# Performance work log

Measured on AMD Instinct MI355X. Metric: run time of the kernel, lower is better.

## Reference

```python
import jax, jax.numpy as jnp
import numpy as np

N = 100000
D_IN = 64
D_HID = 64


def _sage_conv(x, edge_index, Wl, bl, Wr):
    # PyG SAGEConv (mean aggr): out = lin_l(mean_j x_j) + lin_r(x_root)
    src, dst = edge_index[0], edge_index[1]
    n = x.shape[0]
    msg_sum = jax.ops.segment_sum(x[src], dst, num_segments=n)  # [N, d]
    deg = jax.ops.segment_sum(jnp.ones_like(src, dtype=x.dtype), dst, num_segments=n)
    agg = msg_sum / jnp.maximum(deg, 1.0)[:, None]
    return agg @ Wl + bl + x @ Wr


def setup_inputs() -> dict:
    key = jax.random.key(0)
    ks = jax.random.split(key, 8)
    x = jax.random.normal(ks[0], (N, D_IN), dtype=jnp.float32)
    edge_index = jax.random.randint(ks[1], (2, 16 * N), 0, N, dtype=jnp.int64)
    s = 1.0 / np.sqrt(D_IN)
    W1l = jax.random.uniform(ks[2], (D_IN, D_HID), minval=-s, maxval=s, dtype=jnp.float32)
    b1 = jnp.zeros((D_HID,), dtype=jnp.float32)
    W1r = jax.random.uniform(ks[3], (D_IN, D_HID), minval=-s, maxval=s, dtype=jnp.float32)
    s2 = 1.0 / np.sqrt(D_HID)
    W2l = jax.random.uniform(ks[4], (D_HID, D_HID), minval=-s2, maxval=s2, dtype=jnp.float32)
    b2 = jnp.zeros((D_HID,), dtype=jnp.float32)
    W2r = jax.random.uniform(ks[5], (D_HID, D_HID), minval=-s2, maxval=s2, dtype=jnp.float32)
    Wc = jax.random.uniform(ks[6], (D_HID, 2), minval=-s2, maxval=s2, dtype=jnp.float32)
    bc = jax.random.uniform(ks[7], (2,), minval=-s2, maxval=s2, dtype=jnp.float32)
    return {"x": x, "edge_index": edge_index, "W1l": W1l, "b1": b1, "W1r": W1r,
            "W2l": W2l, "b2": b2, "W2r": W2r, "Wc": Wc, "bc": bc}


def reference(x, edge_index, W1l, b1, W1r, W2l, b2, W2r, Wc, bc):
    h = jax.nn.relu(_sage_conv(x, edge_index, W1l, b1, W1r))
    h = _sage_conv(h, edge_index, W2l, b2, W2r)
    return h @ Wc + bc  # [N, 2] logits
```

## Files before the change

### kernel.cpp

```cpp
#include <hip/hip_runtime.h>


#define SCAN_BS 1024
#define BUCKET_BITS 7
#define BUCKET_NODES 128
#define NBUCK_MAX 1024
#define EPB 8192

__global__ void __launch_bounds__(256) bucket_hist_kernel(const int* __restrict__ dst,
                                                          int* __restrict__ counts,
                                                          int ne, int B, int NB) {
  __shared__ int hist[NBUCK_MAX];
  for (int k = threadIdx.x; k < B; k += 256) hist[k] = 0;
  __syncthreads();
  int base = blockIdx.x * EPB;
#pragma unroll 4
  for (int i = 0; i < EPB / 256; ++i) {
    int e = base + i * 256 + threadIdx.x;
    if (e < ne) atomicAdd(&hist[dst[e] >> BUCKET_BITS], 1);
  }
  __syncthreads();
  for (int k = threadIdx.x; k < B; k += 256) counts[k * NB + blockIdx.x] = hist[k];
}

__device__ __forceinline__ int block_scan_inclusive_1024(int v, int* wsums) {
  int lane = threadIdx.x & 63;
  int wid = threadIdx.x >> 6;
  int s = v;
#pragma unroll
  for (int off = 1; off < 64; off <<= 1) {
    int t = __shfl_up(s, off);
    if (lane >= off) s += t;
  }
  if (lane == 63) wsums[wid] = s;
  __syncthreads();
  if (wid == 0) {
    int ws = (lane < 16) ? wsums[lane] : 0;
#pragma unroll
    for (int off = 1; off < 16; off <<= 1) {
      int t = __shfl_up(ws, off);
      if (lane >= off) ws += t;
    }
    if (lane < 16) wsums[lane] = ws;
  }
  __syncthreads();
  if (wid > 0) s += wsums[wid - 1];
  return s;
}

__global__ void __launch_bounds__(SCAN_BS) scan_a_inplace_kernel(int* __restrict__ data,
                                                                 int* __restrict__ bsums,
                                                                 int S) {
  __shared__ int wsums[16];
  int i = blockIdx.x * SCAN_BS + threadIdx.x;
  int v = (i < S) ? data[i] : 0;
  int inc = block_scan_inclusive_1024(v, wsums);
  if (i < S) data[i] = inc - v;
  if (threadIdx.x == SCAN_BS - 1) bsums[blockIdx.x] = inc;
}

__global__ void __launch_bounds__(SCAN_BS) scan_b_kernel(const int* __restrict__ bsums,
                                                         int* __restrict__ boffs, int nb) {
  __shared__ int wsums[16];
  int v = ((int)threadIdx.x < nb) ? bsums[threadIdx.x] : 0;
  int inc = block_scan_inclusive_1024(v, wsums);
  if ((int)threadIdx.x < nb) boffs[threadIdx.x] = inc - v;
  if ((int)threadIdx.x == nb - 1) boffs[nb] = inc;
}

__global__ void add_offs_kernel(int* __restrict__ v, const int* __restrict__ boffs, int S) {
  int i = blockIdx.x * blockDim.x + threadIdx.x;
  if (i < S) v[i] += boffs[i >> 10];
}

__global__ void __launch_bounds__(256) bucket_place_kernel(const int* __restrict__ src,
                                                           const int* __restrict__ dst,
                                                           const int* __restrict__ counts,
                                                           int* __restrict__ arr,
                                                           int ne, int B, int NB) {
  __shared__ int cur[NBUCK_MAX];
  for (int k = threadIdx.x; k < B; k += 256) cur[k] = counts[k * NB + blockIdx.x];
  __syncthreads();
  int base = blockIdx.x * EPB;
#pragma unroll 4
  for (int i = 0; i < EPB / 256; ++i) {
    int e = base + i * 256 + threadIdx.x;
    if (e < ne) {
      int d = dst[e];
      int k = d >> BUCKET_BITS;
      int pos = atomicAdd(&cur[k], 1);
      arr[pos] = (src[e] << BUCKET_BITS) | (d & (BUCKET_NODES - 1));
    }
  }
}

__global__ void __launch_bounds__(256) csr_bucket_kernel(const int* __restrict__ arr,
                                                         const int* __restrict__ counts,
                                                         int* __restrict__ row_ptr,
                                                         int* __restrict__ col,
                                                         int n, int ne, int B, int NB) {
  __shared__ int hist[BUCKET_NODES];
  __shared__ int incl[BUCKET_NODES];
  __shared__ int cur[BUCKET_NODES];
  __shared__ int tot0s;
  int k = blockIdx.x;
  int tid = threadIdx.x;
  int start = counts[k * NB];
  int end = (k + 1 < B) ? counts[(k + 1) * NB] : ne;
  if (tid < BUCKET_NODES) hist[tid] = 0;
  __syncthreads();
  for (int e = start + tid; e < end; e += 256)
    atomicAdd(&hist[arr[e] & (BUCKET_NODES - 1)], 1);
  __syncthreads();
  int lane = tid & 63, wid = tid >> 6;
  if (wid < 2) {
    int s = hist[wid * 64 + lane];
#pragma unroll
    for (int off = 1; off < 64; off <<= 1) {
      int t = __shfl_up(s, off);
      if (lane >= off) s += t;
    }
    incl[wid * 64 + lane] = s;
    if (wid == 0 && lane == 63) tot0s = s;
  }
  __syncthreads();
  if (tid < BUCKET_NODES) {
    int e0 = ((tid & 63) == 0) ? 0 : incl[tid - 1];
    if (tid >= 64) e0 += tot0s;
    int base = start + e0;
    cur[tid] = base;
    int node = k * BUCKET_NODES + tid;
    if (node < n) row_ptr[node] = base;
  }
  if (k == B - 1 && tid == 0) row_ptr[n] = ne;
  __syncthreads();
  for (int e = start + tid; e < end; e += 256) {
    int p = arr[e];
    int pos = atomicAdd(&cur[p & (BUCKET_NODES - 1)], 1);
    col[pos] = p >> BUCKET_BITS;
  }
}

__global__ void __launch_bounds__(256) aggregate_kernel(const float* __restrict__ xin,
                                                        const int* __restrict__ row_ptr,
                                                        const int* __restrict__ col,
                                                        float* __restrict__ outp, int n) {
  int gwave = (blockIdx.x * 256 + threadIdx.x) >> 6;
  int lane = threadIdx.x & 63;
  if (gwave >= n) return;
  int m = __builtin_amdgcn_readfirstlane(gwave);
  int start = row_ptr[m];
  int end = row_ptr[m + 1];
  float a[16];
#pragma unroll
  for (int i = 0; i < 16; ++i) a[i] = 0.f;
  int e = start;
  for (; e + 16 <= end; e += 16) {
    int c[16];
#pragma unroll
    for (int i = 0; i < 16; ++i) c[i] = col[e + i];
#pragma unroll
    for (int i = 0; i < 16; ++i) a[i] += xin[(size_t)c[i] * 64 + lane];
  }
  for (; e + 4 <= end; e += 4) {
    int c0 = col[e + 0], c1 = col[e + 1], c2 = col[e + 2], c3 = col[e + 3];
    a[0] += xin[(size_t)c0 * 64 + lane];
    a[1] += xin[(size_t)c1 * 64 + lane];
    a[2] += xin[(size_t)c2 * 64 + lane];
    a[3] += xin[(size_t)c3 * 64 + lane];
  }
  for (; e < end; ++e) a[0] += xin[(size_t)col[e] * 64 + lane];
#pragma unroll
  for (int i = 8; i > 0; i >>= 1)
#pragma unroll
    for (int j = 0; j < i; ++j) a[j] += a[j + i];
  int d = end - start;
  float inv = 1.0f / (float)((d > 0) ? d : 1);
  outp[(size_t)m * 64 + lane] = a[0] * inv;
}

#define GBM 128

__device__ __forceinline__ void gemm_phase(const float* __restrict__ M,
                                           const float* __restrict__ W,
                                           float (&Mt)[GBM][65], float (&Ws)[64][64],
                                           float4 (&acc)[8],
                                           int node0, int n, int tx, int ty, int t) {
  __syncthreads();
#pragma unroll
  for (int i = 0; i < 8; ++i) {
    int f4 = i * 256 + t;
    int r = f4 >> 4, c4 = f4 & 15;
    int nd = node0 + r;
    float4 v = make_float4(0.f, 0.f, 0.f, 0.f);
    if (nd < n) v = ((const float4*)(M + (size_t)nd * 64))[c4];
    Mt[r][c4 * 4 + 0] = v.x; Mt[r][c4 * 4 + 1] = v.y;
    Mt[r][c4 * 4 + 2] = v.z; Mt[r][c4 * 4 + 3] = v.w;
  }
#pragma unroll
  for (int i = 0; i < 4; ++i) {
    int f4 = i * 256 + t;
    int k = f4 >> 4, c4 = f4 & 15;
    float4 v = ((const float4*)W)[f4];
    *(float4*)&Ws[k][c4 * 4] = v;
  }
  __syncthreads();
#pragma unroll 4
  for (int k = 0; k < 64; ++k) {
    float4 w4 = *(const float4*)&Ws[k][tx * 4];
    float a[8];
#pragma unroll
    for (int m = 0; m < 8; ++m) a[m] = Mt[ty * 8 + m][k];
#pragma unroll
    for (int m = 0; m < 8; ++m) {
      acc[m].x = fmaf(a[m], w4.x, acc[m].x);
      acc[m].y = fmaf(a[m], w4.y, acc[m].y);
      acc[m].z = fmaf(a[m], w4.z, acc[m].z);
      acc[m].w = fmaf(a[m], w4.w, acc[m].w);
    }
  }
}

__global__ void __launch_bounds__(256) gemm_relu_kernel(const float* __restrict__ A,
                                                        const float* __restrict__ X,
                                                        const float* __restrict__ Wl,
                                                        const float* __restrict__ bias,
                                                        const float* __restrict__ Wr,
                                                        float* __restrict__ H, int n) {
  __shared__ float Mt[GBM][65];
  __shared__ float Ws[64][64];
  int t = threadIdx.x;
  int tx = t & 15, ty = t >> 4;
  int node0 = blockIdx.x * GBM;
  float4 bv = *(const float4*)(bias + tx * 4);
  float4 acc[8];
#pragma unroll
  for (int m = 0; m < 8; ++m) acc[m] = bv;
  gemm_phase(A, Wl, Mt, Ws, acc, node0, n, tx, ty, t);
  gemm_phase(X, Wr, Mt, Ws, acc, node0, n, tx, ty, t);
#pragma unroll
  for (int m = 0; m < 8; ++m) {
    int nd = node0 + ty * 8 + m;
    if (nd < n) {
      float4 v;
      v.x = fmaxf(acc[m].x, 0.f);
      v.y = fmaxf(acc[m].y, 0.f);
      v.z = fmaxf(acc[m].z, 0.f);
      v.w = fmaxf(acc[m].w, 0.f);
      ((float4*)(H + (size_t)nd * 64))[tx] = v;
    }
  }
}

__global__ void __launch_bounds__(256) gemm_cls_kernel(const float* __restrict__ A,
                                                       const float* __restrict__ X,
                                                       const float* __restrict__ Wl,
                                                       const float* __restrict__ bias,
                                                       const float* __restrict__ Wr,
                                                       const float* __restrict__ Wc,
                                                       const float* __restrict__ bc,
                                                       float* __restrict__ outp, int n) {
  __shared__ float Mt[GBM][65];
  __shared__ float Ws[64][64];
  int t = threadIdx.x;
  int tx = t & 15, ty = t >> 4;
  int node0 = blockIdx.x * GBM;
  float4 bv = *(const float4*)(bias + tx * 4);
  float4 acc[8];
#pragma unroll
  for (int m = 0; m < 8; ++m) acc[m] = bv;
  gemm_phase(A, Wl, Mt, Ws, acc, node0, n, tx, ty, t);
  gemm_phase(X, Wr, Mt, Ws, acc, node0, n, tx, ty, t);
  float2 wc0 = *(const float2*)(Wc + (tx * 4 + 0) * 2);
  float2 wc1 = *(const float2*)(Wc + (tx * 4 + 1) * 2);
  float2 wc2 = *(const float2*)(Wc + (tx * 4 + 2) * 2);
  float2 wc3 = *(const float2*)(Wc + (tx * 4 + 3) * 2);
  float b0 = bc[0], b1 = bc[1];
#pragma unroll
  for (int m = 0; m < 8; ++m) {
    float p0 = acc[m].x * wc0.x + acc[m].y * wc1.x + acc[m].z * wc2.x + acc[m].w * wc3.x;
    float p1 = acc[m].x * wc0.y + acc[m].y * wc1.y + acc[m].z * wc2.y + acc[m].w * wc3.y;
#pragma unroll
    for (int off = 1; off < 16; off <<= 1) {
      p0 += __shfl_xor(p0, off);
      p1 += __shfl_xor(p1, off);
    }
    if (tx == 0) {
      int nd = node0 + ty * 8 + m;
      if (nd < n) {
        float2 o;
        o.x = p0 + b0;
        o.y = p1 + b1;
        *(float2*)(outp + (size_t)nd * 2) = o;
      }
    }
  }
}

extern "C" void kernel_launch(void* const* d_in, const int* in_sizes, int n_in,
                              void* d_out, int out_size, void* d_ws, size_t ws_size,
                              hipStream_t stream) {
  const float* x   = (const float*)d_in[0];
  const int*   ei  = (const int*)d_in[1];
  const float* W1l = (const float*)d_in[2];
  const float* b1  = (const float*)d_in[3];
  const float* W1r = (const float*)d_in[4];
  const float* W2l = (const float*)d_in[5];
  const float* b2  = (const float*)d_in[6];
  const float* W2r = (const float*)d_in[7];
  const float* Wc  = (const float*)d_in[8];
  const float* bc  = (const float*)d_in[9];
  float* out = (float*)d_out;

  const int n  = in_sizes[0] / 64;
  const int ne = in_sizes[1] / 2;
  const int* src = ei;
  const int* dst = ei + ne;

  const int B  = (n + BUCKET_NODES - 1) >> BUCKET_BITS;
  const int NB = (ne + EPB - 1) / EPB;
  const int S  = B * NB;
  const int nsb = (S + SCAN_BS - 1) / SCAN_BS;

  char* ws = (char*)d_ws;
  size_t off = 0;
  auto carve = [&](size_t bytes) -> void* {
    void* p = ws + off;
    off += (bytes + 255) & ~(size_t)255;
    return p;
  };
  int* counts  = (int*)carve((size_t)S * 4);
  int* bsums   = (int*)carve((size_t)(nsb + 1) * 4);
  int* boffs   = (int*)carve((size_t)(nsb + 1) * 4);
  int* col     = (int*)carve((size_t)ne * 4);
  int* row_ptr = (int*)carve((size_t)(n + 1) * 4);
  float* m1    = (float*)carve((size_t)n * 64 * 4);
  float* h     = (float*)carve((size_t)n * 64 * 4);
  int* arr     = (int*)m1;
  (void)ws_size;

  bucket_hist_kernel<<<NB, 256, 0, stream>>>(dst, counts, ne, B, NB);
  scan_a_inplace_kernel<<<nsb, SCAN_BS, 0, stream>>>(counts, bsums, S);
  scan_b_kernel<<<1, SCAN_BS, 0, stream>>>(bsums, boffs, nsb);
  add_offs_kernel<<<(S + 255) / 256, 256, 0, stream>>>(counts, boffs, S);
  bucket_place_kernel<<<NB, 256, 0, stream>>>(src, dst, counts, arr, ne, B, NB);
  csr_bucket_kernel<<<B, 256, 0, stream>>>(arr, counts, row_ptr, col, n, ne, B, NB);

  const int gtiles = (n + GBM - 1) / GBM;
  aggregate_kernel<<<(n * 64 + 255) / 256, 256, 0, stream>>>(x, row_ptr, col, m1, n);
  gemm_relu_kernel<<<gtiles, 256, 0, stream>>>(m1, x, W1l, b1, W1r, h, n);

  aggregate_kernel<<<(n * 64 + 255) / 256, 256, 0, stream>>>(h, row_ptr, col, m1, n);
  gemm_cls_kernel<<<gtiles, 256, 0, stream>>>(m1, h, W2l, b2, W2r, Wc, bc, out, n);
}
```

Baseline: 327.7 us.

## Widen CSR buckets to 512 nodes and stage column writes in shared memory

Bucket size grows from 128 to 512 nodes, so the bucket count drops to about 196. The csr_bucket kernel now scans two counters per thread with a 256-thread block scan. Scattered column-index writes go to a shared-memory staging buffer first and are then written to global memory in coalesced order, with an overflow path for buckets beyond capacity. This cuts random global writes in the CSR build, but with fewer, larger blocks the GPU may be underfilled and shared-memory use per block is higher.

```diff
diff --git a/kernel.cpp b/kernel.cpp
--- a/kernel.cpp
+++ b/kernel.cpp
@@ -2,10 +2,11 @@
 
 
 #define SCAN_BS 1024
-#define BUCKET_BITS 7
-#define BUCKET_NODES 128
-#define NBUCK_MAX 1024
+#define BUCKET_BITS 9
+#define BUCKET_NODES 512
+#define NBUCK_MAX 256
 #define EPB 8192
+#define STAGE_CAP 10240
 
 __global__ void __launch_bounds__(256) bucket_hist_kernel(const int* __restrict__ dst,
                                                           int* __restrict__ counts,
@@ -45,6 +46,31 @@
   }
   __syncthreads();
   if (wid > 0) s += wsums[wid - 1];
+  return s;
+}
+
+__device__ __forceinline__ int block_scan_inclusive_256(int v, int* wsums4) {
+  int lane = threadIdx.x & 63;
+  int wid = threadIdx.x >> 6;
+  int s = v;
+#pragma unroll
+  for (int off = 1; off < 64; off <<= 1) {
+    int t = __shfl_up(s, off);
+    if (lane >= off) s += t;
+  }
+  if (lane == 63) wsums4[wid] = s;
+  __syncthreads();
+  if (wid == 0) {
+    int ws = (lane < 4) ? wsums4[lane] : 0;
+#pragma unroll
+    for (int off = 1; off < 4; off <<= 1) {
+      int t = __shfl_up(ws, off);
+      if (lane >= off) ws += t;
+    }
+    if (lane < 4) wsums4[lane] = ws;
+  }
+  __syncthreads();
+  if (wid > 0) s += wsums4[wid - 1];
   return s;
 }
 
@@ -100,45 +126,42 @@
                                                          int* __restrict__ col,
                                                          int n, int ne, int B, int NB) {
   __shared__ int hist[BUCKET_NODES];
-  __shared__ int incl[BUCKET_NODES];
   __shared__ int cur[BUCKET_NODES];
-  __shared__ int tot0s;
+  __shared__ int stage[STAGE_CAP];
+  __shared__ int wsums4[4];
   int k = blockIdx.x;
   int tid = threadIdx.x;
   int start = counts[k * NB];
   int end = (k + 1 < B) ? counts[(k + 1) * NB] : ne;
-  if (tid < BUCKET_NODES) hist[tid] = 0;
+  int size = end - start;
+  hist[tid] = 0;
+  hist[tid + 256] = 0;
   __syncthreads();
   for (int e = start + tid; e < end; e += 256)
     atomicAdd(&hist[arr[e] & (BUCKET_NODES - 1)], 1);
   __syncthreads();
-  int lane = tid & 63, wid = tid >> 6;
-  if (wid < 2) {
-    int s = hist[wid * 64 + lane];
-#pragma unroll
-    for (int off = 1; off < 64; off <<= 1) {
-      int t = __shfl_up(s, off);
-      if (lane >= off) s += t;
-    }
-    incl[wid * 64 + lane] = s;
-    if (wid == 0 && lane == 63) tot0s = s;
-  }
-  __syncthreads();
-  if (tid < BUCKET_NODES) {
-    int e0 = ((tid & 63) == 0) ? 0 : incl[tid - 1];
-    if (tid >= 64) e0 += tot0s;
-    int base = start + e0;
-    cur[tid] = base;
-    int node = k * BUCKET_NODES + tid;
-    if (node < n) row_ptr[node] = base;
+  int v0 = hist[tid * 2], v1 = hist[tid * 2 + 1];
+  int inc = block_scan_inclusive_256(v0 + v1, wsums4);
+  int e0 = inc - (v0 + v1);
+  {
+    int node0 = k * BUCKET_NODES;
+    cur[tid * 2] = e0;
+    cur[tid * 2 + 1] = e0 + v0;
+    if (node0 + tid * 2 < n) row_ptr[node0 + tid * 2] = start + e0;
+    if (node0 + tid * 2 + 1 < n) row_ptr[node0 + tid * 2 + 1] = start + e0 + v0;
   }
   if (k == B - 1 && tid == 0) row_ptr[n] = ne;
   __syncthreads();
   for (int e = start + tid; e < end; e += 256) {
     int p = arr[e];
     int pos = atomicAdd(&cur[p & (BUCKET_NODES - 1)], 1);
-    col[pos] = p >> BUCKET_BITS;
-  }
+    int s = p >> BUCKET_BITS;
+    if (pos < STAGE_CAP) stage[pos] = s;
+    else col[start + pos] = s;
+  }
+  __syncthreads();
+  int lim = (size < STAGE_CAP) ? size : STAGE_CAP;
+  for (int i = tid; i < lim; i += 256) col[start + i] = stage[i];
 }
 
 __global__ void __launch_bounds__(256) aggregate_kernel(const float* __restrict__ xin,
```

Result: no change. 329.7 us (+0.6%).
